# Kernel tuning notes

Measured on AMD Instinct MI355X. Metric: run time of the kernel, lower is better.

Reference implementation:

```python
import jax, jax.numpy as jnp
import numpy as np

B, L, HID = 4, 2048, 896
NH, NKV, HD = 14, 2, 64
GROUPS = NH // NKV  # 7
ROPE_THETA = 1000000.0


def _rotate_half(x):
    x1, x2 = x[..., : HD // 2], x[..., HD // 2 :]
    return jnp.concatenate([-x2, x1], axis=-1)


def setup_inputs() -> dict:
    key = jax.random.key(0)
    ks = jax.random.split(key, 8)
    x = jax.random.normal(ks[0], (B, L, HID), dtype=jnp.float32)
    # RoPE tables (HF convention: freqs repeated twice along last dim)
    inv_freq = 1.0 / (ROPE_THETA ** (np.arange(0, HD, 2, dtype=np.float32) / HD))
    t = np.arange(L, dtype=np.float32)
    freqs = np.outer(t, inv_freq)  # [L, HD/2]
    emb = np.concatenate([freqs, freqs], axis=-1)  # [L, HD]
    cos = jnp.asarray(np.cos(emb))[None, None]  # [1,1,L,HD]
    sin = jnp.asarray(np.sin(emb))[None, None]
    # Causal additive mask (finite large negative for numerical safety)
    causal = jnp.tril(jnp.ones((L, L), dtype=bool))
    mask = jnp.where(causal, 0.0, -1e9).astype(jnp.float32)[None, None]
    s = 0.02
    wq = jax.random.normal(ks[1], (NH * HD, HID), dtype=jnp.float32) * s
    bq = jax.random.normal(ks[2], (NH * HD,), dtype=jnp.float32) * s
    wk = jax.random.normal(ks[3], (NKV * HD, HID), dtype=jnp.float32) * s
    bk = jax.random.normal(ks[4], (NKV * HD,), dtype=jnp.float32) * s
    wv = jax.random.normal(ks[5], (NKV * HD, HID), dtype=jnp.float32) * s
    bv = jax.random.normal(ks[6], (NKV * HD,), dtype=jnp.float32) * s
    wo = jax.random.normal(ks[7], (HID, NH * HD), dtype=jnp.float32) * s
    return {"x": x, "cos": cos, "sin": sin, "mask": mask,
            "wq": wq, "bq": bq, "wk": wk, "bk": bk, "wv": wv, "bv": bv, "wo": wo}


def reference(x, cos, sin, mask, wq, bq, wk, bk, wv, bv, wo):
    b, l, _ = x.shape
    q = (x @ wq.T + bq).reshape(b, l, NH, HD).transpose(0, 2, 1, 3)   # [B,NH,L,HD]
    k = (x @ wk.T + bk).reshape(b, l, NKV, HD).transpose(0, 2, 1, 3)  # [B,NKV,L,HD]
    v = (x @ wv.T + bv).reshape(b, l, NKV, HD).transpose(0, 2, 1, 3)
    # RoPE
    q = q * cos + _rotate_half(q) * sin
    k = k * cos + _rotate_half(k) * sin
    # GQA expansion of KV heads
    k = jnp.repeat(k, GROUPS, axis=1)  # [B,NH,L,HD]
    v = jnp.repeat(v, GROUPS, axis=1)
    scale = 1.0 / jnp.sqrt(jnp.float32(HD))
    attn = jnp.einsum("bhqd,bhkd->bhqk", q, k) * scale + mask
    attn = jax.nn.softmax(attn, axis=-1)
    out = jnp.einsum("bhqk,bhkd->bhqd", attn, v)
    out = out.transpose(0, 2, 1, 3).reshape(b, l, NH * HD)
    return out @ wo.T
```

## Files before the change

kernel.cpp:

```cpp
#include <hip/hip_runtime.h>
#include <hip/hip_bf16.h>
#include <math.h>

#define B 4
#define L 2048
#define HID 896
#define NH 14
#define NKV 2
#define HD 64
#define GROUPS 7
#define QCOLS (NH * HD)
#define KCOLS (NKV * HD)
#define ROWS (B * L)
#define QKVS 1152

typedef __attribute__((ext_vector_type(8))) short bf16x8;
typedef __attribute__((ext_vector_type(4))) short bf16x4;
typedef __attribute__((ext_vector_type(4))) float f32x4;
typedef unsigned short ushort_t;
typedef unsigned int uint_t;

__device__ inline short f2bf(float f) {
  union { __hip_bfloat16 h; short s; } u;
  u.h = __float2bfloat16(f);
  return u.s;
}

__device__ inline uint_t pack2_bf16(float a, float b) {
  return (uint_t)(ushort_t)f2bf(a) | ((uint_t)(ushort_t)f2bf(b) << 16);
}

#if defined(__HIP_DEVICE_COMPILE__)
__device__ inline f32x4 mfma16(bf16x4 a, bf16x4 b, f32x4 c) {
  return __builtin_amdgcn_mfma_f32_16x16x16bf16_1k(a, b, c, 0, 0, 0);
}
#define EXP2(x) __builtin_amdgcn_exp2f(x)
#else
__device__ inline f32x4 mfma16(bf16x4 a, bf16x4 b, f32x4 c) { return c; }
#define EXP2(x) exp2f(x)
#endif

__device__ inline void gload_lds16(const void* g, void* l) {
  __builtin_amdgcn_global_load_lds(
      (const __attribute__((address_space(1))) unsigned int*)g,
      (__attribute__((address_space(3))) unsigned int*)l, 16, 0, 0);
}

__device__ inline void cast8(const float* __restrict__ in,
                             short* __restrict__ out) {
  const float4* p = (const float4*)in;
  float4 a = p[0], b = p[1];
  short s[8];
  s[0] = f2bf(a.x); s[1] = f2bf(a.y); s[2] = f2bf(a.z); s[3] = f2bf(a.w);
  s[4] = f2bf(b.x); s[5] = f2bf(b.y); s[6] = f2bf(b.z); s[7] = f2bf(b.w);
  *(bf16x8*)out = *(bf16x8*)s;
}

#define NX8 (ROWS * HID / 8)
#define NQ8 (QCOLS * HID / 8)
#define NK8 (KCOLS * HID / 8)
#define PREP_TOTAL (NX8 + NQ8 + NK8 + NK8 + NQ8 + QKVS)

__global__ void prep_kernel(const float* __restrict__ x,
                            const float* __restrict__ wq,
                            const float* __restrict__ wk,
                            const float* __restrict__ wv,
                            const float* __restrict__ wo,
                            const float* __restrict__ bq,
                            const float* __restrict__ bk,
                            const float* __restrict__ bv,
                            short* __restrict__ xb,
                            short* __restrict__ wqkvb,
                            short* __restrict__ wob,
                            float* __restrict__ bqkv) {
  int i = blockIdx.x * blockDim.x + threadIdx.x;
  if (i < NX8) { cast8(x + (size_t)i * 8, xb + (size_t)i * 8); return; }
  i -= NX8;
  if (i < NQ8) { cast8(wq + (size_t)i * 8, wqkvb + (size_t)i * 8); return; }
  i -= NQ8;
  if (i < NK8) {
    cast8(wk + (size_t)i * 8, wqkvb + (size_t)QCOLS * HID + (size_t)i * 8);
    return;
  }
  i -= NK8;
  if (i < NK8) {
    cast8(wv + (size_t)i * 8,
          wqkvb + (size_t)(QCOLS + KCOLS) * HID + (size_t)i * 8);
    return;
  }
  i -= NK8;
  if (i < NQ8) { cast8(wo + (size_t)i * 8, wob + (size_t)i * 8); return; }
  i -= NQ8;
  if (i < QKVS) {
    float v;
    if (i < QCOLS) v = bq[i];
    else if (i < QCOLS + KCOLS) v = bk[i - QCOLS];
    else v = bv[i - QCOLS - KCOLS];
    bqkv[i] = v;
  }
}

#define GTM 128
#define GTN 128
#define GTK 32
#define QSCALE 0.18033688011112042f

template <bool ROPE>
__global__ __launch_bounds__(256) void gemm_bf16_kernel(
    const short* __restrict__ A, const short* __restrict__ W,
    const float* __restrict__ bias, float* __restrict__ C,
    short* __restrict__ Cb, const float* __restrict__ cosp,
    const float* __restrict__ sinp, int M, int N, int K) {
  __shared__ short As[GTM * GTK];
  __shared__ short Bs[GTN * GTK];

  const int tid = threadIdx.x;
  const int wave = tid >> 6;
  const int lane = tid & 63;
  const int l15 = lane & 15;
  const int quad = lane >> 4;
  const int m0 = blockIdx.y * GTM;
  const int n0 = blockIdx.x * GTN;
  const int wm = (wave >> 1) * 64;
  const int wn = (wave & 1) * 64;

  f32x4 acc[4][4] = {};

  const int c0 = tid, c1 = tid + 256;
  const int r0 = c0 >> 2, g0 = (c0 & 3) ^ ((r0 >> 1) & 3);
  const int r1 = c1 >> 2, g1 = (c1 & 3) ^ ((r1 >> 1) & 3);
  const short* Ag0 = A + (size_t)(m0 + r0) * K + g0 * 8;
  const short* Ag1 = A + (size_t)(m0 + r1) * K + g1 * 8;
  const short* Wg0 = W + (size_t)(n0 + r0) * K + g0 * 8;
  const short* Wg1 = W + (size_t)(n0 + r1) * K + g1 * 8;

  const int goff = ((quad ^ ((l15 >> 1) & 3)) * 8);

  for (int k0 = 0; k0 < K; k0 += GTK) {
    __syncthreads();
    gload_lds16(Ag0 + k0, As + c0 * 8);
    gload_lds16(Ag1 + k0, As + c1 * 8);
    gload_lds16(Wg0 + k0, Bs + c0 * 8);
    gload_lds16(Wg1 + k0, Bs + c1 * 8);
    __syncthreads();

    bf16x8 af[4], bfr[4];
#pragma unroll
    for (int i = 0; i < 4; ++i)
      af[i] = *(bf16x8*)(As + (wm + i * 16 + l15) * GTK + goff);
#pragma unroll
    for (int j = 0; j < 4; ++j)
      bfr[j] = *(bf16x8*)(Bs + (wn + j * 16 + l15) * GTK + goff);
#pragma unroll
    for (int i = 0; i < 4; ++i)
#pragma unroll
      for (int j = 0; j < 4; ++j)
        acc[i][j] = __builtin_amdgcn_mfma_f32_16x16x32_bf16(af[i], bfr[j],
                                                            acc[i][j], 0, 0, 0);
  }

  const int col0 = n0 + wn + l15;
  if (ROPE) {
    const int hw = (n0 + wn) >> 6;
    float bv[4];
#pragma unroll
    for (int j = 0; j < 4; ++j) bv[j] = bias[col0 + 16 * j];
    if (hw < NH + NKV) {
      const float sc = (hw < NH) ? QSCALE : 1.0f;
#pragma unroll
      for (int i = 0; i < 4; ++i) {
        const int rowb = m0 + wm + i * 16 + quad * 4;
#pragma unroll
        for (int r = 0; r < 4; ++r) {
          const int row = rowb + r;
          const int l = row & (L - 1);
          const float* cp = cosp + l * HD + l15;
          const float* sp = sinp + l * HD + l15;
#pragma unroll
          for (int j = 0; j < 2; ++j) {
            const float cv = cp[16 * j];
            const float sv = sp[16 * j];
            const float a = acc[i][j][r] + bv[j];
            const float b2 = acc[i][j + 2][r] + bv[j + 2];
            Cb[(size_t)row * N + col0 + 16 * j] = f2bf((a * cv - b2 * sv) * sc);
            Cb[(size_t)row * N + col0 + 16 * j + 32] =
                f2bf((b2 * cv + a * sv) * sc);
          }
        }
      }
    } else {
#pragma unroll
      for (int j = 0; j < 4; ++j)
#pragma unroll
        for (int i = 0; i < 4; ++i) {
          const int rowb = m0 + wm + i * 16 + quad * 4;
#pragma unroll
          for (int r = 0; r < 4; ++r)
            Cb[(size_t)(rowb + r) * N + col0 + 16 * j] =
                f2bf(acc[i][j][r] + bv[j]);
        }
    }
  } else {
#pragma unroll
    for (int j = 0; j < 4; ++j) {
      const int col = col0 + 16 * j;
      const float bv = bias ? bias[col] : 0.f;
#pragma unroll
      for (int i = 0; i < 4; ++i) {
        const int rowb = m0 + wm + i * 16 + quad * 4;
#pragma unroll
        for (int r = 0; r < 4; ++r)
          C[(size_t)(rowb + r) * N + col] = acc[i][j][r] + bv;
      }
    }
  }
}

#define BK 64
#define QSTRIP 128
#define NSTRIPS (L / QSTRIP)

__global__ __launch_bounds__(512, 4) void attn_mfma_kernel(
    const ushort_t* __restrict__ qkv, ushort_t* __restrict__ ctx) {
  const int strip = (NSTRIPS - 1) - blockIdx.y;
  const int h = blockIdx.x % NH;
  const int b = blockIdx.x / NH;
  const int kvh = h / GROUPS;
  const int tid = threadIdx.x;
  const int wave = tid >> 6;
  const int lane = tid & 63;
  const int l15 = lane & 15;
  const int quad = lane >> 4;

  const int lt = 2 * strip + 1;
  const int qrb = strip * QSTRIP + wave * 16;
  const int myDiag = (qrb + 15) >> 6;

  __shared__ short Kt[2][BK * 64];
  __shared__ short Vt[2][BK * 64];

  bf16x8 qf[2];
  {
    const ushort_t* qp = qkv + (size_t)(b * L + qrb + l15) * QKVS + h * HD;
    qf[0] = *(const bf16x8*)(qp + quad * 8);
    qf[1] = *(const bf16x8*)(qp + 32 + quad * 8);
  }

  float m = -INFINITY, lsum = 0.f;
  f32x4 o[4] = {};

  const ushort_t* kb = qkv + (size_t)(b * L) * QKVS + QCOLS + kvh * HD;
  const ushort_t* vb = kb + KCOLS;

  const int skey = tid >> 3;
  const int sgr = tid & 7;
  const int ksw = skey * 64 + (sgr ^ (skey & 7)) * 8;
  const int vd = tid & 63;
  const int vsw = vd * 64 + ((wave ^ (vd & 7)) * 8);

  uint4 kr, vrp;

  auto load_tile = [&](int j0) {
    kr = *(const uint4*)(kb + (size_t)(j0 + skey) * QKVS + sgr * 8);
    const ushort_t* vp = vb + (size_t)(j0 + wave * 8) * QKVS + vd;
    ushort_t vr[8];
#pragma unroll
    for (int s2 = 0; s2 < 8; ++s2) vr[s2] = vp[(size_t)s2 * QKVS];
    vrp.x = (uint_t)vr[0] | ((uint_t)vr[1] << 16);
    vrp.y = (uint_t)vr[2] | ((uint_t)vr[3] << 16);
    vrp.z = (uint_t)vr[4] | ((uint_t)vr[5] << 16);
    vrp.w = (uint_t)vr[6] | ((uint_t)vr[7] << 16);
  };
  auto store_tile = [&](int bufi) {
    *(uint4*)(&Kt[bufi][ksw]) = kr;
    *(uint4*)(&Vt[bufi][vsw]) = vrp;
  };

  load_tile(0);
  store_tile(0);
  __syncthreads();

  const int dl7 = l15 & 7;
  const int qh = quad >> 1;
  const int qoff = (quad & 1) * 4;

  for (int t = 0; t <= lt; ++t) {
    const int j0 = t * BK;
    const int cur = t & 1;
    if (t < lt) load_tile(j0 + BK);

    if (t <= myDiag) {
      const short* Kb = Kt[cur];
      const short* Vb = Vt[cur];

      f32x4 St[4];
      __builtin_amdgcn_s_setprio(1);
#pragma unroll
      for (int tt = 0; tt < 4; ++tt) {
        const int key = tt * 16 + l15;
        const short* krow = Kb + key * 64;
        bf16x8 k0 = *(const bf16x8*)(krow + (quad ^ (key & 7)) * 8);
        bf16x8 k1 = *(const bf16x8*)(krow + ((4 + quad) ^ (key & 7)) * 8);
        f32x4 a = {};
        a = __builtin_amdgcn_mfma_f32_16x16x32_bf16(k0, qf[0], a, 0, 0, 0);
        a = __builtin_amdgcn_mfma_f32_16x16x32_bf16(k1, qf[1], a, 0, 0, 0);
        St[tt] = a;
      }
      __builtin_amdgcn_s_setprio(0);

      float s[16];
      if (t == myDiag) {
        const int limq = qrb + l15 - j0 - quad * 4;
#pragma unroll
        for (int tt = 0; tt < 4; ++tt)
#pragma unroll
          for (int r = 0; r < 4; ++r)
            s[tt * 4 + r] = (tt * 16 + r <= limq) ? St[tt][r] : -1e30f;
      } else {
#pragma unroll
        for (int tt = 0; tt < 4; ++tt)
#pragma unroll
          for (int r = 0; r < 4; ++r) s[tt * 4 + r] = St[tt][r];
      }

      float mt = fmaxf(s[0], s[1]);
#pragma unroll
      for (int i = 2; i < 16; ++i) mt = fmaxf(mt, s[i]);
      float pl[16], psl = 0.f;
#pragma unroll
      for (int i = 0; i < 16; ++i) {
        pl[i] = EXP2(s[i] - mt);
        psl += pl[i];
      }
      float mg = fmaxf(mt, __shfl_xor(mt, 16));
      mg = fmaxf(mg, __shfl_xor(mg, 32));

      float f;
      if (__all(mg <= m + 8.0f)) {
        f = EXP2(mt - m);
        lsum += psl * f;
      } else {
        const float mn = fmaxf(m, mg);
        const float al = EXP2(m - mn);
        f = EXP2(mt - mn);
        m = mn;
        lsum = lsum * al + psl * f;
#pragma unroll
        for (int c = 0; c < 4; ++c)
#pragma unroll
          for (int r = 0; r < 4; ++r) o[c][r] *= al;
      }

      uint_t pk[8];
#pragma unroll
      for (int tt = 0; tt < 4; ++tt) {
        pk[2 * tt] = pack2_bf16(pl[4 * tt] * f, pl[4 * tt + 1] * f);
        pk[2 * tt + 1] = pack2_bf16(pl[4 * tt + 2] * f, pl[4 * tt + 3] * f);
      }

      __builtin_amdgcn_s_setprio(1);
#pragma unroll
      for (int c = 0; c < 4; ++c) {
        const short* vrow = Vb + (c * 16 + l15) * 64;
#pragma unroll
        for (int tt = 0; tt < 4; ++tt) {
          const int g = tt * 2 + qh;
          union { bf16x4 v; uint2 u; } vfu;
          vfu.u = *(const uint2*)(vrow + ((g ^ dl7) * 8) + qoff);
          union { bf16x4 v; uint_t u[2]; } pa;
          pa.u[0] = pk[2 * tt];
          pa.u[1] = pk[2 * tt + 1];
          o[c] = mfma16(vfu.v, pa.v, o[c]);
        }
      }
      __builtin_amdgcn_s_setprio(0);
    }

    if (t < lt) store_tile(cur ^ 1);
    __syncthreads();
  }

  float s1 = lsum;
  s1 += __shfl_xor(s1, 16);
  s1 += __shfl_xor(s1, 32);
  const float inv = 1.0f / s1;
  ushort_t* cb = ctx + (size_t)(b * L) * QCOLS + h * HD;
#pragma unroll
  for (int c = 0; c < 4; ++c) {
    uint_t w[2];
    w[0] = pack2_bf16(o[c][0] * inv, o[c][1] * inv);
    w[1] = pack2_bf16(o[c][2] * inv, o[c][3] * inv);
    *(uint2*)(cb + (size_t)(qrb + l15) * QCOLS + c * 16 + quad * 4) =
        *(uint2*)w;
  }
}

extern "C" void kernel_launch(void* const* d_in, const int* in_sizes, int n_in,
                              void* d_out, int out_size, void* d_ws,
                              size_t ws_size, hipStream_t stream) {
  const float* x = (const float*)d_in[0];
  const float* cosp = (const float*)d_in[1];
  const float* sinp = (const float*)d_in[2];
  const float* wq = (const float*)d_in[4];
  const float* bq = (const float*)d_in[5];
  const float* wk = (const float*)d_in[6];
  const float* bk = (const float*)d_in[7];
  const float* wv = (const float*)d_in[8];
  const float* bv = (const float*)d_in[9];
  const float* wo = (const float*)d_in[10];
  float* out = (float*)d_out;

  char* ws = (char*)d_ws;
  ushort_t* qkvb = (ushort_t*)ws;
  ws += (size_t)ROWS * QKVS * 2;
  short* xb = (short*)ws;
  ws += (size_t)ROWS * HID * 2;
  short* wqkvb = (short*)ws;
  ws += (size_t)QKVS * HID * 2;
  short* wob = (short*)ws;
  ws += (size_t)HID * QCOLS * 2;
  ushort_t* ctxb = (ushort_t*)ws;
  ws += (size_t)ROWS * QCOLS * 2;
  float* bqkv = (float*)ws;
  ws += QKVS * 4;

  prep_kernel<<<(PREP_TOTAL + 255) / 256, 256, 0, stream>>>(
      x, wq, wk, wv, wo, bq, bk, bv, xb, wqkvb, wob, bqkv);

  gemm_bf16_kernel<true><<<dim3(QKVS / GTN, ROWS / GTM), 256, 0, stream>>>(
      xb, wqkvb, bqkv, nullptr, (short*)qkvb, cosp, sinp, ROWS, QKVS, HID);

  attn_mfma_kernel<<<dim3(NH * B, NSTRIPS), 512, 0, stream>>>(qkvb, ctxb);

  gemm_bf16_kernel<false><<<dim3(HID / GTN, ROWS / GTM), 256, 0, stream>>>(
      (const short*)ctxb, wob, nullptr, out, nullptr, nullptr, nullptr, ROWS,
      HID, QCOLS);
}
```

Baseline: 238.3 us.

## Pre-transpose V in separate kernel and stage K/V tiles via direct global-to-LDS loads

```diff
diff --git a/kernel.cpp b/kernel.cpp
--- a/kernel.cpp
+++ b/kernel.cpp
@@ -216,12 +216,47 @@
   }
 }
 
+__global__ __launch_bounds__(256) void vtrans_kernel(
+    const ushort_t* __restrict__ qkv, ushort_t* __restrict__ vt) {
+  const int j0 = blockIdx.x * 64;
+  const int kvh = blockIdx.y;
+  const int b = blockIdx.z;
+  const int t = threadIdx.x;
+  __shared__ short Vs[64 * 64];
+
+  const ushort_t* src =
+      qkv + (size_t)(b * L) * QKVS + QCOLS + KCOLS + kvh * HD;
+  {
+    const int k0 = t >> 3, p = t & 7;
+    const int k1 = k0 + 32;
+    gload_lds16(src + (size_t)(j0 + k0) * QKVS + ((p ^ (k0 & 7)) * 8),
+                Vs + t * 8);
+    gload_lds16(src + (size_t)(j0 + k1) * QKVS + ((p ^ (k1 & 7)) * 8),
+                Vs + (t + 256) * 8);
+  }
+  __syncthreads();
+
+  const int d = t >> 2;
+  const int kk0 = (t & 3) * 16;
+  ushort_t outv[16];
+#pragma unroll
+  for (int k = 0; k < 16; ++k) {
+    const int key = kk0 + k;
+    outv[k] =
+        (ushort_t)Vs[key * 64 + (((d >> 3) ^ (key & 7)) * 8) + (d & 7)];
+  }
+  ushort_t* dst = vt + ((size_t)(b * NKV + kvh) * 64 + d) * L + j0 + kk0;
+  *(uint4*)dst = *(uint4*)outv;
+  *(uint4*)(dst + 8) = *(uint4*)(outv + 8);
+}
+
 #define BK 64
 #define QSTRIP 128
 #define NSTRIPS (L / QSTRIP)
 
 __global__ __launch_bounds__(512, 4) void attn_mfma_kernel(
-    const ushort_t* __restrict__ qkv, ushort_t* __restrict__ ctx) {
+    const ushort_t* __restrict__ qkv, const ushort_t* __restrict__ vt,
+    ushort_t* __restrict__ ctx) {
   const int strip = (NSTRIPS - 1) - blockIdx.y;
   const int h = blockIdx.x % NH;
   const int b = blockIdx.x / NH;
@@ -250,34 +285,19 @@
   f32x4 o[4] = {};
 
   const ushort_t* kb = qkv + (size_t)(b * L) * QKVS + QCOLS + kvh * HD;
-  const ushort_t* vb = kb + KCOLS;
-
-  const int skey = tid >> 3;
-  const int sgr = tid & 7;
-  const int ksw = skey * 64 + (sgr ^ (skey & 7)) * 8;
-  const int vd = tid & 63;
-  const int vsw = vd * 64 + ((wave ^ (vd & 7)) * 8);
-
-  uint4 kr, vrp;
-
-  auto load_tile = [&](int j0) {
-    kr = *(const uint4*)(kb + (size_t)(j0 + skey) * QKVS + sgr * 8);
-    const ushort_t* vp = vb + (size_t)(j0 + wave * 8) * QKVS + vd;
-    ushort_t vr[8];
-#pragma unroll
-    for (int s2 = 0; s2 < 8; ++s2) vr[s2] = vp[(size_t)s2 * QKVS];
-    vrp.x = (uint_t)vr[0] | ((uint_t)vr[1] << 16);
-    vrp.y = (uint_t)vr[2] | ((uint_t)vr[3] << 16);
-    vrp.z = (uint_t)vr[4] | ((uint_t)vr[5] << 16);
-    vrp.w = (uint_t)vr[6] | ((uint_t)vr[7] << 16);
+  const ushort_t* vtb = vt + (size_t)(b * NKV + kvh) * 64 * L;
+
+  const int srow = tid >> 3;
+  const int sgl = (tid & 7) ^ (srow & 7);
+  const ushort_t* ksrc = kb + (size_t)srow * QKVS + sgl * 8;
+  const ushort_t* vsrc = vtb + (size_t)srow * L + sgl * 8;
+
+  auto stage = [&](int j0, int bufi) {
+    gload_lds16(ksrc + (size_t)j0 * QKVS, &Kt[bufi][tid * 8]);
+    gload_lds16(vsrc + j0, &Vt[bufi][tid * 8]);
   };
-  auto store_tile = [&](int bufi) {
-    *(uint4*)(&Kt[bufi][ksw]) = kr;
-    *(uint4*)(&Vt[bufi][vsw]) = vrp;
-  };
-
-  load_tile(0);
-  store_tile(0);
+
+  stage(0, 0);
   __syncthreads();
 
   const int dl7 = l15 & 7;
@@ -287,7 +307,7 @@
   for (int t = 0; t <= lt; ++t) {
     const int j0 = t * BK;
     const int cur = t & 1;
-    if (t < lt) load_tile(j0 + BK);
+    if (t < lt) stage(j0 + BK, cur ^ 1);
 
     if (t <= myDiag) {
       const short* Kb = Kt[cur];
@@ -376,7 +396,6 @@
       __builtin_amdgcn_s_setprio(0);
     }
 
-    if (t < lt) store_tile(cur ^ 1);
     __syncthreads();
   }
 
@@ -421,6 +440,8 @@
   ws += (size_t)HID * QCOLS * 2;
   ushort_t* ctxb = (ushort_t*)ws;
   ws += (size_t)ROWS * QCOLS * 2;
+  ushort_t* vtb = (ushort_t*)ws;
+  ws += (size_t)B * NKV * 64 * L * 2;
   float* bqkv = (float*)ws;
   ws += QKVS * 4;
 
@@ -430,7 +451,9 @@
   gemm_bf16_kernel<true><<<dim3(QKVS / GTN, ROWS / GTM), 256, 0, stream>>>(
       xb, wqkvb, bqkv, nullptr, (short*)qkvb, cosp, sinp, ROWS, QKVS, HID);
 
-  attn_mfma_kernel<<<dim3(NH * B, NSTRIPS), 512, 0, stream>>>(qkvb, ctxb);
+  vtrans_kernel<<<dim3(L / 64, NKV, B), 256, 0, stream>>>(qkvb, vtb);
+
+  attn_mfma_kernel<<<dim3(NH * B, NSTRIPS), 512, 0, stream>>>(qkvb, vtb, ctxb);
 
   gemm_bf16_kernel<false><<<dim3(HID / GTN, ROWS / GTM), 256, 0, stream>>>(
       (const short*)ctxb, wob, nullptr, out, nullptr, nullptr, nullptr, ROWS,
```

New measurement: 240.4 us. Within noise of the previous version (+0.9%).
